# Kernel tuning notes

Hardware: AMD Instinct MI355X
Metric: run time of the kernel (lower is better)

The kernel has to match this reference:

```python
import jax, jax.numpy as jnp
import numpy as np


def conv1x1(x, w, b):
    # x: [B,Cin,H,W], w: [Cout,Cin], b: [Cout]
    return jnp.einsum('bchw,oc->bohw', x, w) + b[None, :, None, None]


def setup_inputs() -> dict:
    key = jax.random.key(0)
    ks = jax.random.split(key, 10)
    B, Cm, C, H, W = 4, 6, 64, 64, 64
    map1 = jax.random.normal(ks[0], (B, Cm, H, W), jnp.float32)
    map2 = jax.random.normal(ks[1], (B, Cm, H, W), jnp.float32)
    feature_map = jax.random.normal(ks[2], (B, C, H, W), jnp.float32)
    # 1x1 conv params (kaiming-ish scale)
    wb = jax.random.normal(ks[3], (Cm, Cm), jnp.float32) / np.sqrt(Cm)
    bb = jnp.zeros((Cm,), jnp.float32)
    wc = jax.random.normal(ks[4], (Cm, Cm), jnp.float32) / np.sqrt(Cm)
    bc = jnp.zeros((Cm,), jnp.float32)
    wd = jax.random.normal(ks[5], (C, C), jnp.float32) / np.sqrt(C)
    bd = jnp.zeros((C,), jnp.float32)
    alpha = jnp.zeros((1,), jnp.float32)
    return {"map1": map1, "map2": map2, "feature_map": feature_map,
            "wb": wb, "bb": bb, "wc": wc, "bc": bc, "wd": wd, "bd": bd,
            "alpha": alpha}


def reference(map1, map2, feature_map, wb, bb, wc, bc, wd, bd, alpha):
    B, _, H, W = map1.shape
    N = H * W
    # conv1x1 projections, flatten spatial
    feat_b = conv1x1(map1, wb, bb).reshape(B, -1, N).transpose(0, 2, 1)  # [B,N,6]
    feat_c = conv1x1(map2, wc, bc).reshape(B, -1, N)                      # [B,6,N]
    attention_s = jax.nn.softmax(jnp.einsum('bnc,bcm->bnm', feat_b, feat_c), axis=-1)  # [B,N,N]
    feat_d = conv1x1(feature_map, wd, bd).reshape(B, -1, N)               # [B,C,N]
    # bmm with attention_s^T: out[b,c,n] = sum_m feat_d[b,c,m] * attn[b,n,m]
    feat_e = jnp.einsum('bcm,bnm->bcn', feat_d, attention_s).reshape(B, -1, H, W)
    return alpha * feat_e + feature_map
```

## Files before the change

kernel.cpp:

```cpp
#include <hip/hip_runtime.h>
#include <hip/hip_bf16.h>
#include <math.h>


#define BATCH 4
#define CMAP  6
#define CH    64
#define NSP   4096
#define TN    64
#define NTH   32

typedef __attribute__((ext_vector_type(8))) short short8;
typedef __attribute__((ext_vector_type(4))) float f32x4;

#if __has_builtin(__builtin_amdgcn_exp2f)
#define EXP2(x) __builtin_amdgcn_exp2f(x)
#else
#define EXP2(x) exp2f(x)
#endif

__device__ __forceinline__ unsigned f2bf(float f) {
    unsigned u = __float_as_uint(f);
    return (u + 0x7fffu + ((u >> 16) & 1u)) >> 16;
}

#define INVLN2 1.44269504088896f
#define SHIFT_BF16 0xC238u
#define ONE_BF16   0x3F80u


__global__ void proj_kernel(const float* __restrict__ map1, const float* __restrict__ map2,
                            const float* __restrict__ fm,
                            const float* __restrict__ wb, const float* __restrict__ bb,
                            const float* __restrict__ wc, const float* __restrict__ bc,
                            const float* __restrict__ wd, const float* __restrict__ bd,
                            unsigned short* __restrict__ featq8,
                            unsigned short* __restrict__ featk8,
                            unsigned short* __restrict__ featdf)
{
    __shared__ unsigned short vfrag[2048];

    const int b    = blockIdx.z;
    const int half = blockIdx.y;
    const int lane = threadIdx.x & 63;
    const int og   = threadIdx.x >> 6;
    const int n    = blockIdx.x * 64 + lane;

    const int ht = lane >> 5;
    const int mm = lane & 31;
    const int q4 = mm >> 3, jj = mm & 7;
    const int cb_local = og >> 1;
    float vals[CH];
#pragma unroll
    for (int c = 0; c < CH; ++c)
        vals[c] = fm[(size_t)(b*CH + c)*NSP + n];
#pragma unroll
    for (int oi = 0; oi < 8; ++oi) {
        const int o = half*32 + og*8 + oi;
        float a = bd[o];
#pragma unroll
        for (int c = 0; c < CH; ++c)
            a = fmaf(vals[c], wd[o*CH + c], a);
        const int r = (og & 1)*8 + oi;
        vfrag[(ht*2 + cb_local)*512 + (q4*16 + r)*8 + jj] = (unsigned short)f2bf(a);
    }

    if (half == 0 && og == 0) {
        float v1[CMAP], v2[CMAP];
#pragma unroll
        for (int c = 0; c < CMAP; ++c) {
            v1[c] = map1[(size_t)(b*CMAP + c)*NSP + n];
            v2[c] = map2[(size_t)(b*CMAP + c)*NSP + n];
        }
        unsigned qv[CMAP], kv[CMAP];
#pragma unroll
        for (int o = 0; o < CMAP; ++o) {
            float a1 = bb[o], a2 = bc[o];
#pragma unroll
            for (int c = 0; c < CMAP; ++c) {
                a1 = fmaf(v1[c], wb[o*CMAP + c], a1);
                a2 = fmaf(v2[c], wc[o*CMAP + c], a2);
            }
            qv[o] = f2bf(a1 * INVLN2);
            kv[o] = f2bf(a2);
        }
        uint4 qw, kw;
        qw.x = qv[0] | (qv[1] << 16);
        qw.y = qv[2] | (qv[3] << 16);
        qw.z = qv[4] | (qv[5] << 16);
        qw.w = SHIFT_BF16;
        kw.x = kv[0] | (kv[1] << 16);
        kw.y = kv[2] | (kv[3] << 16);
        kw.z = kv[4] | (kv[5] << 16);
        kw.w = ONE_BF16;
        *(uint4*)&featq8[(size_t)(b*NSP + n)*8] = qw;
        *(uint4*)&featk8[(size_t)(b*NSP + n)*8] = kw;
    }

    __syncthreads();

    {
        const int tt = threadIdx.x;
        const uint4 d = *(const uint4*)&vfrag[tt*8];
        const int ht2 = tt >> 7, inner = tt & 127;
        const size_t off = (((size_t)(b*128 + blockIdx.x*2 + ht2)*4) + half*2)*512
                         + (size_t)inner*8;
        *(uint4*)&featdf[off] = d;
    }
}

__global__ __launch_bounds__(256, 2)
void attn_kernel(const unsigned short* __restrict__ featq8,
                 const unsigned short* __restrict__ featk8,
                 const unsigned short* __restrict__ featdf,
                 const float* __restrict__ fm, const float* __restrict__ alpha_p,
                 float* __restrict__ out)
{
    __shared__ float cmb[2][64][20];

    const int b    = blockIdx.y;
    const int t    = threadIdx.x;
    const int lane = t & 63, w = t >> 6;
    const int row16 = lane & 15, quad = lane >> 4;
    const int qsub  = w >> 1;
    const int khalf = w & 1;
    const int n0w  = blockIdx.x * 32 + qsub * 16;
    const int m0   = khalf * (NSP/2);

    short8 qf = {0,0,0,0,0,0,0,0};
    if (quad == 0)
        qf = *(const short8*)&featq8[(size_t)(b*NSP + n0w + row16)*8];

    const short8 onesA = {(short)ONE_BF16,(short)ONE_BF16,(short)ONE_BF16,(short)ONE_BF16,
                          (short)ONE_BF16,(short)ONE_BF16,(short)ONE_BF16,(short)ONE_BF16};

    const int perm16 = ((row16 >> 2) << 3) + (row16 & 3);
    const unsigned short* kbase = featk8 + ((size_t)(b*NSP + m0) + perm16)*8 + quad*8;
    const unsigned short* vfb = featdf + ((size_t)b*128*4)*512 + lane*8;
    const int hb = khalf * 64;

    const f32x4 zf = {0.f,0.f,0.f,0.f};
    f32x4 acc[4] = {zf, zf, zf, zf};
    f32x4 accL = zf;

#define LOADK(mt)                                                               \
    kc0 = *(const short8*)(kbase + ((mt)*TN +  0)*8);                           \
    kc1 = *(const short8*)(kbase + ((mt)*TN +  4)*8);                           \
    kc2 = *(const short8*)(kbase + ((mt)*TN + 32)*8);                           \
    kc3 = *(const short8*)(kbase + ((mt)*TN + 36)*8);

#define LOADV(vt)                                                               \
    vv0 = *(const short8*)(vfb + (size_t)((hb + (vt)*2 + 0)*4 + 0)*512);        \
    vv1 = *(const short8*)(vfb + (size_t)((hb + (vt)*2 + 1)*4 + 0)*512);        \
    vv2 = *(const short8*)(vfb + (size_t)((hb + (vt)*2 + 0)*4 + 1)*512);        \
    vv3 = *(const short8*)(vfb + (size_t)((hb + (vt)*2 + 1)*4 + 1)*512);        \
    vv4 = *(const short8*)(vfb + (size_t)((hb + (vt)*2 + 0)*4 + 2)*512);        \
    vv5 = *(const short8*)(vfb + (size_t)((hb + (vt)*2 + 1)*4 + 2)*512);        \
    vv6 = *(const short8*)(vfb + (size_t)((hb + (vt)*2 + 0)*4 + 3)*512);        \
    vv7 = *(const short8*)(vfb + (size_t)((hb + (vt)*2 + 1)*4 + 3)*512);

#define SCORES(d0, d1, d2, d3)                                                  \
    d0 = __builtin_amdgcn_mfma_f32_16x16x32_bf16(kc0, qf, zf, 0, 0, 0);         \
    d1 = __builtin_amdgcn_mfma_f32_16x16x32_bf16(kc1, qf, zf, 0, 0, 0);         \
    d2 = __builtin_amdgcn_mfma_f32_16x16x32_bf16(kc2, qf, zf, 0, 0, 0);         \
    d3 = __builtin_amdgcn_mfma_f32_16x16x32_bf16(kc3, qf, zf, 0, 0, 0);

#define EXPPACK                                                                 \
    {                                                                           \
        const float e0 = EXP2(sp0[0]), e1 = EXP2(sp0[1]);                       \
        const float e2 = EXP2(sp0[2]), e3 = EXP2(sp0[3]);                       \
        const float e4 = EXP2(sp1[0]), e5 = EXP2(sp1[1]);                       \
        const float e6 = EXP2(sp1[2]), e7 = EXP2(sp1[3]);                       \
        const float e8 = EXP2(sp2[0]), e9 = EXP2(sp2[1]);                       \
        const float ea = EXP2(sp2[2]), eb = EXP2(sp2[3]);                       \
        const float ec = EXP2(sp3[0]), ed = EXP2(sp3[1]);                       \
        const float ee = EXP2(sp3[2]), ef = EXP2(sp3[3]);                       \
        uint4 u0, u1;                                                           \
        u0.x = __builtin_amdgcn_perm(__float_as_uint(e1), __float_as_uint(e0), 0x07060302u); \
        u0.y = __builtin_amdgcn_perm(__float_as_uint(e3), __float_as_uint(e2), 0x07060302u); \
        u0.z = __builtin_amdgcn_perm(__float_as_uint(e5), __float_as_uint(e4), 0x07060302u); \
        u0.w = __builtin_amdgcn_perm(__float_as_uint(e7), __float_as_uint(e6), 0x07060302u); \
        u1.x = __builtin_amdgcn_perm(__float_as_uint(e9), __float_as_uint(e8), 0x07060302u); \
        u1.y = __builtin_amdgcn_perm(__float_as_uint(eb), __float_as_uint(ea), 0x07060302u); \
        u1.z = __builtin_amdgcn_perm(__float_as_uint(ed), __float_as_uint(ec), 0x07060302u); \
        u1.w = __builtin_amdgcn_perm(__float_as_uint(ef), __float_as_uint(ee), 0x07060302u); \
        pb0 = *(short8*)&u0;                                                    \
        pb1 = *(short8*)&u1;                                                    \
    }

#define PVALL                                                                   \
    acc[0] = __builtin_amdgcn_mfma_f32_16x16x32_bf16(vv0, pb0, acc[0], 0, 0, 0); \
    acc[0] = __builtin_amdgcn_mfma_f32_16x16x32_bf16(vv1, pb1, acc[0], 0, 0, 0); \
    acc[1] = __builtin_amdgcn_mfma_f32_16x16x32_bf16(vv2, pb0, acc[1], 0, 0, 0); \
    acc[1] = __builtin_amdgcn_mfma_f32_16x16x32_bf16(vv3, pb1, acc[1], 0, 0, 0); \
    acc[2] = __builtin_amdgcn_mfma_f32_16x16x32_bf16(vv4, pb0, acc[2], 0, 0, 0); \
    acc[2] = __builtin_amdgcn_mfma_f32_16x16x32_bf16(vv5, pb1, acc[2], 0, 0, 0); \
    acc[3] = __builtin_amdgcn_mfma_f32_16x16x32_bf16(vv6, pb0, acc[3], 0, 0, 0); \
    acc[3] = __builtin_amdgcn_mfma_f32_16x16x32_bf16(vv7, pb1, acc[3], 0, 0, 0); \
    accL   = __builtin_amdgcn_mfma_f32_16x16x32_bf16(onesA, pb0, accL, 0, 0, 0); \
    accL   = __builtin_amdgcn_mfma_f32_16x16x32_bf16(onesA, pb1, accL, 0, 0, 0);

    short8 kc0, kc1, kc2, kc3;
    short8 vv0, vv1, vv2, vv3, vv4, vv5, vv6, vv7;
    short8 pb0, pb1;
    f32x4 sp0, sp1, sp2, sp3;

    LOADK(0)
    SCORES(sp0, sp1, sp2, sp3)
    LOADK(1)
    LOADV(0)

    for (int i = 1; i < NTH; ++i) {
        f32x4 t0, t1, t2, t3;
        SCORES(t0, t1, t2, t3)
        LOADK(i + 1)

        EXPPACK
        PVALL

        LOADV(i)
        sp0 = t0; sp1 = t1; sp2 = t2; sp3 = t3;
    }

    EXPPACK
    PVALL
#undef LOADK
#undef LOADV
#undef SCORES
#undef EXPPACK
#undef PVALL

    if (khalf == 1) {
        float* c = cmb[qsub][lane];
#pragma unroll
        for (int cb = 0; cb < 4; ++cb)
            *(float4*)&c[cb*4] = (float4){acc[cb][0], acc[cb][1], acc[cb][2], acc[cb][3]};
        c[16] = accL[0];
    }
    __syncthreads();
    if (khalf == 0) {
        const float* c = cmb[qsub][lane];
        const float alpha = alpha_p[0];
        const float cinv = alpha / (accL[0] + c[16] + 1e-30f);
        const int n = n0w + row16;
#pragma unroll
        for (int cb = 0; cb < 4; ++cb) {
            const float4 po = *(const float4*)&c[cb*4];
            const float pv[4] = {po.x, po.y, po.z, po.w};
#pragma unroll
            for (int r = 0; r < 4; ++r) {
                const int ch = cb*16 + quad*4 + r;
                const size_t idx = (size_t)(b*CH + ch)*NSP + n;
                out[idx] = fmaf(cinv, acc[cb][r] + pv[r], fm[idx]);
            }
        }
    }
}

extern "C" void kernel_launch(void* const* d_in, const int* in_sizes, int n_in,
                              void* d_out, int out_size, void* d_ws, size_t ws_size,
                              hipStream_t stream)
{
    const float* map1  = (const float*)d_in[0];
    const float* map2  = (const float*)d_in[1];
    const float* fm    = (const float*)d_in[2];
    const float* wb    = (const float*)d_in[3];
    const float* bb    = (const float*)d_in[4];
    const float* wc    = (const float*)d_in[5];
    const float* bc    = (const float*)d_in[6];
    const float* wd    = (const float*)d_in[7];
    const float* bd    = (const float*)d_in[8];
    const float* alpha = (const float*)d_in[9];
    float* out = (float*)d_out;

    unsigned short* featq8 = (unsigned short*)d_ws;
    unsigned short* featk8 = featq8 + (size_t)BATCH*NSP*8;
    unsigned short* featdf = featk8 + (size_t)BATCH*NSP*8;

    proj_kernel<<<dim3(NSP/64, 2, BATCH), 256, 0, stream>>>(
        map1, map2, fm, wb, bb, wc, bc, wd, bd, featq8, featk8, featdf);
    attn_kernel<<<dim3(NSP/32, BATCH), 256, 0, stream>>>(
        featq8, featk8, featdf, fm, alpha, out);
}
```

Measured before the change: 119.5 us.

## Split key range across four waves, each covering both query sub-tiles

Before, each pair of waves split the key range in halves for a single 16-query sub-tile. Now each of the four waves takes a quarter of the keys and processes both 16-query sub-tiles, reusing each loaded K and V fragment for two query tiles. The aim is to halve K/V global loads per block. The cost is twice the accumulator and score registers per wave and a three-way LDS reduction into wave 0, which could lower occupancy or spill.

Result: faster. 108.2 us (-9.4%).

```diff
diff --git a/kernel.cpp b/kernel.cpp
--- a/kernel.cpp
+++ b/kernel.cpp
@@ -8,7 +8,7 @@
 #define CH    64
 #define NSP   4096
 #define TN    64
-#define NTH   32
+#define NTQ   16
 
 typedef __attribute__((ext_vector_type(8))) short short8;
 typedef __attribute__((ext_vector_type(4))) float f32x4;
@@ -116,20 +116,20 @@
                  const float* __restrict__ fm, const float* __restrict__ alpha_p,
                  float* __restrict__ out)
 {
-    __shared__ float cmb[2][64][20];
+    __shared__ float cmb[3][64][36];
 
     const int b    = blockIdx.y;
     const int t    = threadIdx.x;
     const int lane = t & 63, w = t >> 6;
     const int row16 = lane & 15, quad = lane >> 4;
-    const int qsub  = w >> 1;
-    const int khalf = w & 1;
-    const int n0w  = blockIdx.x * 32 + qsub * 16;
-    const int m0   = khalf * (NSP/2);
-
-    short8 qf = {0,0,0,0,0,0,0,0};
-    if (quad == 0)
-        qf = *(const short8*)&featq8[(size_t)(b*NSP + n0w + row16)*8];
+    const int n0   = blockIdx.x * 32;
+    const int m0   = w * (NSP/4);
+
+    short8 qf0 = {0,0,0,0,0,0,0,0}, qf1 = {0,0,0,0,0,0,0,0};
+    if (quad == 0) {
+        qf0 = *(const short8*)&featq8[(size_t)(b*NSP + n0 + row16)*8];
+        qf1 = *(const short8*)&featq8[(size_t)(b*NSP + n0 + 16 + row16)*8];
+    }
 
     const short8 onesA = {(short)ONE_BF16,(short)ONE_BF16,(short)ONE_BF16,(short)ONE_BF16,
                           (short)ONE_BF16,(short)ONE_BF16,(short)ONE_BF16,(short)ONE_BF16};
@@ -137,92 +137,90 @@
     const int perm16 = ((row16 >> 2) << 3) + (row16 & 3);
     const unsigned short* kbase = featk8 + ((size_t)(b*NSP + m0) + perm16)*8 + quad*8;
     const unsigned short* vfb = featdf + ((size_t)b*128*4)*512 + lane*8;
-    const int hb = khalf * 64;
+    const int hb = w * 32;
 
     const f32x4 zf = {0.f,0.f,0.f,0.f};
-    f32x4 acc[4] = {zf, zf, zf, zf};
-    f32x4 accL = zf;
+    f32x4 acc[8] = {zf,zf,zf,zf,zf,zf,zf,zf};
+    f32x4 accL2[2] = {zf, zf};
+    f32x4 sp[8];
+    short8 kc[4], vv[8], pb[4];
 
 #define LOADK(mt)                                                               \
-    kc0 = *(const short8*)(kbase + ((mt)*TN +  0)*8);                           \
-    kc1 = *(const short8*)(kbase + ((mt)*TN +  4)*8);                           \
-    kc2 = *(const short8*)(kbase + ((mt)*TN + 32)*8);                           \
-    kc3 = *(const short8*)(kbase + ((mt)*TN + 36)*8);
+    kc[0] = *(const short8*)(kbase + ((mt)*TN +  0)*8);                         \
+    kc[1] = *(const short8*)(kbase + ((mt)*TN +  4)*8);                         \
+    kc[2] = *(const short8*)(kbase + ((mt)*TN + 32)*8);                         \
+    kc[3] = *(const short8*)(kbase + ((mt)*TN + 36)*8);
 
 #define LOADV(vt)                                                               \
-    vv0 = *(const short8*)(vfb + (size_t)((hb + (vt)*2 + 0)*4 + 0)*512);        \
-    vv1 = *(const short8*)(vfb + (size_t)((hb + (vt)*2 + 1)*4 + 0)*512);        \
-    vv2 = *(const short8*)(vfb + (size_t)((hb + (vt)*2 + 0)*4 + 1)*512);        \
-    vv3 = *(const short8*)(vfb + (size_t)((hb + (vt)*2 + 1)*4 + 1)*512);        \
-    vv4 = *(const short8*)(vfb + (size_t)((hb + (vt)*2 + 0)*4 + 2)*512);        \
-    vv5 = *(const short8*)(vfb + (size_t)((hb + (vt)*2 + 1)*4 + 2)*512);        \
-    vv6 = *(const short8*)(vfb + (size_t)((hb + (vt)*2 + 0)*4 + 3)*512);        \
-    vv7 = *(const short8*)(vfb + (size_t)((hb + (vt)*2 + 1)*4 + 3)*512);
-
-#define SCORES(d0, d1, d2, d3)                                                  \
-    d0 = __builtin_amdgcn_mfma_f32_16x16x32_bf16(kc0, qf, zf, 0, 0, 0);         \
-    d1 = __builtin_amdgcn_mfma_f32_16x16x32_bf16(kc1, qf, zf, 0, 0, 0);         \
-    d2 = __builtin_amdgcn_mfma_f32_16x16x32_bf16(kc2, qf, zf, 0, 0, 0);         \
-    d3 = __builtin_amdgcn_mfma_f32_16x16x32_bf16(kc3, qf, zf, 0, 0, 0);
-
-#define EXPPACK                                                                 \
+    _Pragma("unroll")                                                           \
+    for (int cb = 0; cb < 4; ++cb) {                                            \
+        vv[cb*2+0] = *(const short8*)(vfb + (size_t)((hb + (vt)*2 + 0)*4 + cb)*512); \
+        vv[cb*2+1] = *(const short8*)(vfb + (size_t)((hb + (vt)*2 + 1)*4 + cb)*512); \
+    }
+
+#define SCORES(dst)                                                             \
+    _Pragma("unroll")                                                           \
+    for (int kr = 0; kr < 4; ++kr) {                                            \
+        dst[kr]   = __builtin_amdgcn_mfma_f32_16x16x32_bf16(kc[kr], qf0, zf, 0, 0, 0); \
+        dst[4+kr] = __builtin_amdgcn_mfma_f32_16x16x32_bf16(kc[kr], qf1, zf, 0, 0, 0); \
+    }
+
+#define EXPPACK(g)                                                              \
     {                                                                           \
-        const float e0 = EXP2(sp0[0]), e1 = EXP2(sp0[1]);                       \
-        const float e2 = EXP2(sp0[2]), e3 = EXP2(sp0[3]);                       \
-        const float e4 = EXP2(sp1[0]), e5 = EXP2(sp1[1]);                       \
-        const float e6 = EXP2(sp1[2]), e7 = EXP2(sp1[3]);                       \
-        const float e8 = EXP2(sp2[0]), e9 = EXP2(sp2[1]);                       \
-        const float ea = EXP2(sp2[2]), eb = EXP2(sp2[3]);                       \
-        const float ec = EXP2(sp3[0]), ed = EXP2(sp3[1]);                       \
-        const float ee = EXP2(sp3[2]), ef = EXP2(sp3[3]);                       \
+        float e[16];                                                            \
+        _Pragma("unroll")                                                       \
+        for (int u = 0; u < 4; ++u) {                                           \
+            e[u*4+0] = EXP2(sp[(g)*4+u][0]);                                    \
+            e[u*4+1] = EXP2(sp[(g)*4+u][1]);                                    \
+            e[u*4+2] = EXP2(sp[(g)*4+u][2]);                                    \
+            e[u*4+3] = EXP2(sp[(g)*4+u][3]);                                    \
+        }                                                                       \
         uint4 u0, u1;                                                           \
-        u0.x = __builtin_amdgcn_perm(__float_as_uint(e1), __float_as_uint(e0), 0x07060302u); \
-        u0.y = __builtin_amdgcn_perm(__float_as_uint(e3), __float_as_uint(e2), 0x07060302u); \
-        u0.z = __builtin_amdgcn_perm(__float_as_uint(e5), __float_as_uint(e4), 0x07060302u); \
-        u0.w = __builtin_amdgcn_perm(__float_as_uint(e7), __float_as_uint(e6), 0x07060302u); \
-        u1.x = __builtin_amdgcn_perm(__float_as_uint(e9), __float_as_uint(e8), 0x07060302u); \
-        u1.y = __builtin_amdgcn_perm(__float_as_uint(eb), __float_as_uint(ea), 0x07060302u); \
-        u1.z = __builtin_amdgcn_perm(__float_as_uint(ed), __float_as_uint(ec), 0x07060302u); \
-        u1.w = __builtin_amdgcn_perm(__float_as_uint(ef), __float_as_uint(ee), 0x07060302u); \
-        pb0 = *(short8*)&u0;                                                    \
-        pb1 = *(short8*)&u1;                                                    \
+        u0.x = __builtin_amdgcn_perm(__float_as_uint(e[1]),  __float_as_uint(e[0]),  0x07060302u); \
+        u0.y = __builtin_amdgcn_perm(__float_as_uint(e[3]),  __float_as_uint(e[2]),  0x07060302u); \
+        u0.z = __builtin_amdgcn_perm(__float_as_uint(e[5]),  __float_as_uint(e[4]),  0x07060302u); \
+        u0.w = __builtin_amdgcn_perm(__float_as_uint(e[7]),  __float_as_uint(e[6]),  0x07060302u); \
+        u1.x = __builtin_amdgcn_perm(__float_as_uint(e[9]),  __float_as_uint(e[8]),  0x07060302u); \
+        u1.y = __builtin_amdgcn_perm(__float_as_uint(e[11]), __float_as_uint(e[10]), 0x07060302u); \
+        u1.z = __builtin_amdgcn_perm(__float_as_uint(e[13]), __float_as_uint(e[12]), 0x07060302u); \
+        u1.w = __builtin_amdgcn_perm(__float_as_uint(e[15]), __float_as_uint(e[14]), 0x07060302u); \
+        pb[(g)*2+0] = *(short8*)&u0;                                            \
+        pb[(g)*2+1] = *(short8*)&u1;                                            \
     }
 
 #define PVALL                                                                   \
-    acc[0] = __builtin_amdgcn_mfma_f32_16x16x32_bf16(vv0, pb0, acc[0], 0, 0, 0); \
-    acc[0] = __builtin_amdgcn_mfma_f32_16x16x32_bf16(vv1, pb1, acc[0], 0, 0, 0); \
-    acc[1] = __builtin_amdgcn_mfma_f32_16x16x32_bf16(vv2, pb0, acc[1], 0, 0, 0); \
-    acc[1] = __builtin_amdgcn_mfma_f32_16x16x32_bf16(vv3, pb1, acc[1], 0, 0, 0); \
-    acc[2] = __builtin_amdgcn_mfma_f32_16x16x32_bf16(vv4, pb0, acc[2], 0, 0, 0); \
-    acc[2] = __builtin_amdgcn_mfma_f32_16x16x32_bf16(vv5, pb1, acc[2], 0, 0, 0); \
-    acc[3] = __builtin_amdgcn_mfma_f32_16x16x32_bf16(vv6, pb0, acc[3], 0, 0, 0); \
-    acc[3] = __builtin_amdgcn_mfma_f32_16x16x32_bf16(vv7, pb1, acc[3], 0, 0, 0); \
-    accL   = __builtin_amdgcn_mfma_f32_16x16x32_bf16(onesA, pb0, accL, 0, 0, 0); \
-    accL   = __builtin_amdgcn_mfma_f32_16x16x32_bf16(onesA, pb1, accL, 0, 0, 0);
-
-    short8 kc0, kc1, kc2, kc3;
-    short8 vv0, vv1, vv2, vv3, vv4, vv5, vv6, vv7;
-    short8 pb0, pb1;
-    f32x4 sp0, sp1, sp2, sp3;
+    _Pragma("unroll")                                                           \
+    for (int g = 0; g < 2; ++g) {                                               \
+        _Pragma("unroll")                                                       \
+        for (int cb = 0; cb < 4; ++cb) {                                        \
+            acc[g*4+cb] = __builtin_amdgcn_mfma_f32_16x16x32_bf16(vv[cb*2+0], pb[g*2+0], acc[g*4+cb], 0, 0, 0); \
+            acc[g*4+cb] = __builtin_amdgcn_mfma_f32_16x16x32_bf16(vv[cb*2+1], pb[g*2+1], acc[g*4+cb], 0, 0, 0); \
+        }                                                                       \
+        accL2[g] = __builtin_amdgcn_mfma_f32_16x16x32_bf16(onesA, pb[g*2+0], accL2[g], 0, 0, 0); \
+        accL2[g] = __builtin_amdgcn_mfma_f32_16x16x32_bf16(onesA, pb[g*2+1], accL2[g], 0, 0, 0); \
+    }
 
     LOADK(0)
-    SCORES(sp0, sp1, sp2, sp3)
+    SCORES(sp)
     LOADK(1)
     LOADV(0)
 
-    for (int i = 1; i < NTH; ++i) {
-        f32x4 t0, t1, t2, t3;
-        SCORES(t0, t1, t2, t3)
+    for (int i = 1; i < NTQ; ++i) {
+        f32x4 tt[8];
+        SCORES(tt)
         LOADK(i + 1)
 
-        EXPPACK
+        EXPPACK(0)
+        EXPPACK(1)
         PVALL
 
         LOADV(i)
-        sp0 = t0; sp1 = t1; sp2 = t2; sp3 = t3;
-    }
-
-    EXPPACK
+#pragma unroll
+        for (int u = 0; u < 8; ++u) sp[u] = tt[u];
+    }
+
+    EXPPACK(0)
+    EXPPACK(1)
     PVALL
 #undef LOADK
 #undef LOADV
@@ -230,28 +228,42 @@
 #undef EXPPACK
 #undef PVALL
 
-    if (khalf == 1) {
-        float* c = cmb[qsub][lane];
-#pragma unroll
-        for (int cb = 0; cb < 4; ++cb)
-            *(float4*)&c[cb*4] = (float4){acc[cb][0], acc[cb][1], acc[cb][2], acc[cb][3]};
-        c[16] = accL[0];
+    if (w != 0) {
+        float* c = cmb[w - 1][lane];
+#pragma unroll
+        for (int i = 0; i < 8; ++i)
+            *(float4*)&c[i*4] = (float4){acc[i][0], acc[i][1], acc[i][2], acc[i][3]};
+        c[32] = accL2[0][0];
+        c[33] = accL2[1][0];
     }
     __syncthreads();
-    if (khalf == 0) {
-        const float* c = cmb[qsub][lane];
+    if (w == 0) {
+        float l0 = accL2[0][0], l1 = accL2[1][0];
+#pragma unroll
+        for (int ww = 0; ww < 3; ++ww) {
+            const float* c = cmb[ww][lane];
+#pragma unroll
+            for (int i = 0; i < 8; ++i) {
+                const float4 po = *(const float4*)&c[i*4];
+                acc[i][0] += po.x; acc[i][1] += po.y;
+                acc[i][2] += po.z; acc[i][3] += po.w;
+            }
+            l0 += c[32];
+            l1 += c[33];
+        }
         const float alpha = alpha_p[0];
-        const float cinv = alpha / (accL[0] + c[16] + 1e-30f);
-        const int n = n0w + row16;
-#pragma unroll
-        for (int cb = 0; cb < 4; ++cb) {
-            const float4 po = *(const float4*)&c[cb*4];
-            const float pv[4] = {po.x, po.y, po.z, po.w};
-#pragma unroll
-            for (int r = 0; r < 4; ++r) {
-                const int ch = cb*16 + quad*4 + r;
-                const size_t idx = (size_t)(b*CH + ch)*NSP + n;
-                out[idx] = fmaf(cinv, acc[cb][r] + pv[r], fm[idx]);
+        const float cinv[2] = { alpha / (l0 + 1e-30f), alpha / (l1 + 1e-30f) };
+#pragma unroll
+        for (int g = 0; g < 2; ++g) {
+            const int n = n0 + g*16 + row16;
+#pragma unroll
+            for (int cb = 0; cb < 4; ++cb) {
+#pragma unroll
+                for (int r = 0; r < 4; ++r) {
+                    const int ch = cb*16 + quad*4 + r;
+                    const size_t idx = (size_t)(b*CH + ch)*NSP + n;
+                    out[idx] = fmaf(cinv[g], acc[g*4+cb][r], fm[idx]);
+                }
             }
         }
     }
```
